# Performance work log

Hardware: AMD Instinct MI355X
Metric: run time of the kernel (lower is better)

## Reference

```python
import jax, jax.numpy as jnp
import numpy as np

N = 100000          # number of nodes
E = 128             # embedding size
NUM_LAYERS = 4
SMOOTH = 12.0       # MAXIMUM_SMOOTHNESS
RELATIONS = [("at", 2), ("clear", 1), ("on", 2)]  # sorted, as in module
ATOM_COUNTS = {"at": 150000, "clear": 150000, "on": 150000}


def mish(x):
    return x * jnp.tanh(jax.nn.softplus(x))


def _linear_init(k, din, dout):
    s = 1.0 / np.sqrt(din)
    kw, kb = jax.random.split(k)
    w = jax.random.uniform(kw, (din, dout), jnp.float32, -s, s)
    b = jax.random.uniform(kb, (dout,), jnp.float32, -s, s)
    return w, b


def setup_inputs() -> dict:
    key = jax.random.key(0)
    ks = iter(jax.random.split(key, 64))
    inp = {}
    inp["node_embeddings"] = jax.random.normal(next(ks), (N, E), jnp.float32)
    for name, ar in RELATIONS:
        inp[f"atoms_{name}"] = jax.random.randint(
            next(ks), (ATOM_COUNTS[name] * ar,), 0, N, dtype=jnp.int32)
        d = ar * E
        inp[f"w_in_{name}"], inp[f"b_in_{name}"] = _linear_init(next(ks), d, d)
        inp[f"w_out_{name}"], inp[f"b_out_{name}"] = _linear_init(next(ks), d, d)
    # update MLP: Linear(2E, 2E) -> mish -> Linear(2E, E)
    inp["w_u_in"], inp["b_u_in"] = _linear_init(next(ks), 2 * E, 2 * E)
    inp["w_u_out"], inp["b_u_out"] = _linear_init(next(ks), 2 * E, E)
    return inp


def _forward(node_embeddings, atoms, params):
    w_u_in, b_u_in, w_u_out, b_u_out = params["update"]

    def layer(h):
        msgs, idxs = [], []
        for name, ar in RELATIONS:
            w_in, b_in, w_out, b_out = params[name]
            av = atoms[name]                              # [A*ar] node indices
            x = h[av].reshape(-1, ar * E)                 # gather -> [A, ar*E]
            y = x + (mish(x @ w_in + b_in) @ w_out + b_out)  # residual MLP
            msgs.append(y.reshape(-1, E))
            idxs.append(av)
        msg = jnp.concatenate(msgs, 0)                    # [T, E]
        idx = jnp.concatenate(idxs, 0)                    # [T]
        # smooth-max aggregation (max offsets are not differentiated)
        seg_max = jax.ops.segment_max(msg, idx, num_segments=N)
        seg_max = jnp.where(jnp.isfinite(seg_max), seg_max, 0.0)  # empty -> 0 (include_self=False on zeros)
        seg_max = jax.lax.stop_gradient(seg_max)
        exps = jnp.exp(SMOOTH * (msg - seg_max[idx]))
        exps_sum = jax.ops.segment_sum(exps, idx, num_segments=N) + 1e-16
        max_msg = jnp.log(exps_sum) / SMOOTH + seg_max
        upd_in = jnp.concatenate([max_msg, h], axis=1)    # [N, 2E]
        upd = mish(upd_in @ w_u_in + b_u_in) @ w_u_out + b_u_out
        return h + upd                                    # outer residual

    h = node_embeddings
    for _ in range(NUM_LAYERS):
        h = layer(h)
    return h


def reference(node_embeddings, atoms_at, atoms_clear, atoms_on,
              w_in_at, b_in_at, w_out_at, b_out_at,
              w_in_clear, b_in_clear, w_out_clear, b_out_clear,
              w_in_on, b_in_on, w_out_on, b_out_on,
              w_u_in, b_u_in, w_u_out, b_u_out):
    atoms = {"at": atoms_at, "clear": atoms_clear, "on": atoms_on}
    params = {
        "at": (w_in_at, b_in_at, w_out_at, b_out_at),
        "clear": (w_in_clear, b_in_clear, w_out_clear, b_out_clear),
        "on": (w_in_on, b_in_on, w_out_on, b_out_on),
        "update": (w_u_in, b_u_in, w_u_out, b_u_out),
    }
    return _forward(node_embeddings, atoms, params)
```

## Files before the change

### kernel.cpp

```cpp
#include <hip/hip_runtime.h>
#include <hip/hip_bf16.h>
#include <math.h>

#define NNODES 100000
#define EDIM 128
#define TSLOTS 750000
#define NB 391
#define GRA 2344

typedef __bf16 bf16x8 __attribute__((ext_vector_type(8)));
typedef __bf16 bf16x4 __attribute__((ext_vector_type(4)));
typedef float f32x4 __attribute__((ext_vector_type(4)));

#define T_SCALE 17.312340490667562f
#define INV_SCALE 0.05776226504666211f
#define EMPTY_V (-3.0701134f)

__device__ __forceinline__ float mishf(float x) {
  float u = __expf(fminf(x, 15.f));
  float num = u * (u + 2.f);
  return x * num * __builtin_amdgcn_rcpf(num + 2.f);
}

__device__ __forceinline__ double exp12t(float t) {
  t = fmaxf(t, -20000.f);
  float ti = floorf(t);
  float m = exp2f(t - ti);
  int ei = (int)ti;
  ei = ei < -1000 ? -1000 : (ei > 1000 ? 1000 : ei);
  return (double)m * __longlong_as_double(((long long)(1023 + ei)) << 52);
}

__device__ __forceinline__ float logS12(double S) {
  if (!(S > 0.0)) return EMPTY_V;
  long long b = __double_as_longlong(S);
  int e2 = (int)((b >> 52) & 0x7FF) - 1023;
  float mf = __uint_as_float(0x3F800000u | (unsigned)((b >> 29) & 0x7FFFFF));
  return ((float)e2 + log2f(mf)) * INV_SCALE;
}

__global__ void k_sentinel(float* out, int n) {
  int i = blockIdx.x * 256 + threadIdx.x;
  if (i < n) out[i] = 1.0e6f;
}

__global__ void k_init(const float* __restrict__ h0, __bf16* __restrict__ hb, int n8) {
  int i = blockIdx.x * 256 + threadIdx.x;
  if (i >= n8) return;
  float4 f0 = ((const float4*)h0)[i * 2];
  float4 f1 = ((const float4*)h0)[i * 2 + 1];
  bf16x8 p = {(__bf16)f0.x, (__bf16)f0.y, (__bf16)f0.z, (__bf16)f0.w,
              (__bf16)f1.x, (__bf16)f1.y, (__bf16)f1.z, (__bf16)f1.w};
  *(bf16x8*)(hb + (size_t)i * 8) = p;
}

struct TransDesc {
  const float* src[8];
  __bf16* dst[8];
  int R[8];
  int C[8];
  int tstart[9];
};

__global__ void k_transpose_all(TransDesc td) {
  __shared__ float tile[32][33];
  int b = blockIdx.x;
  int m = 0;
  while (m < 7 && b >= td.tstart[m + 1]) m++;
  int t = b - td.tstart[m];
  int R = td.R[m], C = td.C[m];
  int tcols = C >> 5;
  int by = t / tcols, bx = t - by * tcols;
  int tx = threadIdx.x & 31, ty = threadIdx.x >> 5;
  const float* src = td.src[m];
  __bf16* dst = td.dst[m];
  for (int i = 0; i < 32; i += 8)
    tile[ty + i][tx] = src[(size_t)(by * 32 + ty + i) * C + bx * 32 + tx];
  __syncthreads();
  for (int i = 0; i < 32; i += 8)
    dst[(size_t)(bx * 32 + ty + i) * R + by * 32 + tx] = (__bf16)tile[tx][ty + i];
}

__device__ __forceinline__ int slot_node(int s, const int* at, const int* cl, const int* on) {
  if (s < 300000) return at[s];
  if (s < 450000) return cl[s - 300000];
  return on[s - 450000];
}

__global__ void k_count(const int* __restrict__ at, const int* __restrict__ cl,
                        const int* __restrict__ on, int* __restrict__ cnt) {
  int s = blockIdx.x * 256 + threadIdx.x;
  if (s >= TSLOTS) return;
  atomicAdd(&cnt[slot_node(s, at, cl, on)], 1);
}

__global__ void k_bsum(const int* __restrict__ cnt, int* __restrict__ bsum) {
  __shared__ int sm[256];
  int n = blockIdx.x * 256 + threadIdx.x;
  sm[threadIdx.x] = (n < NNODES) ? cnt[n] : 0;
  __syncthreads();
  for (int st = 128; st > 0; st >>= 1) {
    if (threadIdx.x < st) sm[threadIdx.x] += sm[threadIdx.x + st];
    __syncthreads();
  }
  if (threadIdx.x == 0) bsum[blockIdx.x] = sm[0];
}

__global__ void k_bscan(const int* __restrict__ bsum, int* __restrict__ bpre,
                        int* __restrict__ off) {
  __shared__ int sm[512];
  int t = threadIdx.x;
  int v = (t < NB) ? bsum[t] : 0;
  sm[t] = v;
  __syncthreads();
  for (int st = 1; st < 512; st <<= 1) {
    int x = (t >= st) ? sm[t - st] : 0;
    __syncthreads();
    sm[t] += x;
    __syncthreads();
  }
  if (t < NB) bpre[t] = sm[t] - v;
  if (t == NB - 1) off[NNODES] = sm[t];
}

__global__ void k_off(const int* __restrict__ cnt, const int* __restrict__ bpre,
                      int* __restrict__ off) {
  __shared__ int sm[256];
  int n = blockIdx.x * 256 + threadIdx.x;
  int v = (n < NNODES) ? cnt[n] : 0;
  sm[threadIdx.x] = v;
  __syncthreads();
  for (int st = 1; st < 256; st <<= 1) {
    int t = (threadIdx.x >= st) ? sm[threadIdx.x - st] : 0;
    __syncthreads();
    sm[threadIdx.x] += t;
    __syncthreads();
  }
  if (n < NNODES) off[n] = bpre[blockIdx.x] + sm[threadIdx.x] - v;
}

__global__ void k_fill(const int* __restrict__ at, const int* __restrict__ cl,
                       const int* __restrict__ on, const int* __restrict__ off,
                       int* __restrict__ cnt, int* __restrict__ perm) {
  int s = blockIdx.x * 256 + threadIdx.x;
  if (s >= TSLOTS) return;
  int node = slot_node(s, at, cl, on);
  int pos = atomicAdd(&cnt[node], -1) - 1;
  perm[s] = off[node] + pos;
}

struct RelAll {
  const int* av[3];
  const __bf16* wt1[3];
  const float* b1[3];
  const __bf16* wt2[3];
  const float* b2[3];
  const int* prm[3];
};

__global__ __launch_bounds__(512, 6) void k_relf(
    const float* __restrict__ hf, const __bf16* __restrict__ hb,
    RelAll ra, _Float16* __restrict__ msg) {
  __shared__ __align__(16) __bf16 xs[64][264];
  __shared__ int prm[128];
  const int tid = threadIdx.x;
  const int lane = tid & 63;
  const int w = tid >> 6;
  const int b = blockIdx.x;
  const int m = (b < GRA) ? 0 : (b < 2 * GRA ? 1 : 2);
  const int row0 = (b - m * GRA) * 64;
  const int A = 150000;
  const int* av = ra.av[m];
  const __bf16* wt1 = ra.wt1[m];
  const float* b1 = ra.b1[m];
  const __bf16* wt2 = ra.wt2[m];
  const float* b2 = ra.b2[m];
  const int* permrel = ra.prm[m];
  const int lhi = lane >> 4, llo = lane & 15;
  ushort* zs = (ushort*)&xs[0][0];

  if (m < 2) {
    if (tid < 128) {
      int i2 = row0 * 2 + tid;
      prm[tid] = (i2 < 2 * A) ? permrel[i2] : 0;
    }
    if (hb != nullptr) {
      for (int i = 0; i < 4; ++i) {
        int s = tid + i * 512;
        int r = s >> 5, o = s & 31;
        int a = row0 + r;
        uint4 v = {0, 0, 0, 0};
        if (a < A) {
          int node = av[2 * a + (o >> 4)];
          v = *(const uint4*)(hb + (size_t)node * 128 + (o & 15) * 8);
        }
        *(uint4*)&xs[r][o * 8] = v;
      }
    } else {
      for (int i = 0; i < 8; ++i) {
        int s = tid + i * 512;
        int r = s >> 6, o = s & 63;
        int a = row0 + r;
        float4 f = {0.f, 0.f, 0.f, 0.f};
        if (a < A) {
          int node = av[2 * a + (o >> 5)];
          f = *(const float4*)(hf + (size_t)node * 128 + (o & 31) * 4);
        }
        bf16x4 p = {(__bf16)f.x, (__bf16)f.y, (__bf16)f.z, (__bf16)f.w};
        *(bf16x4*)&xs[r][o * 4] = p;
      }
    }
    __syncthreads();

    const int cb = w * 32;
    f32x4 acc1[4][2];
#pragma unroll
    for (int rt = 0; rt < 4; rt++)
#pragma unroll
      for (int ct = 0; ct < 2; ct++) acc1[rt][ct] = (f32x4){0.f, 0.f, 0.f, 0.f};
#pragma unroll
    for (int kk = 0; kk < 8; ++kk) {
      int k = kk * 32 + lhi * 8;
      bf16x8 af[4], bfr[2];
#pragma unroll
      for (int rt = 0; rt < 4; rt++) af[rt] = *(const bf16x8*)&xs[rt * 16 + llo][k];
#pragma unroll
      for (int ct = 0; ct < 2; ct++)
        bfr[ct] = *(const bf16x8*)(wt1 + (size_t)(cb + ct * 16 + llo) * 256 + k);
#pragma unroll
      for (int rt = 0; rt < 4; rt++)
#pragma unroll
        for (int ct = 0; ct < 2; ct++)
          acc1[rt][ct] = __builtin_amdgcn_mfma_f32_16x16x32_bf16(af[rt], bfr[ct], acc1[rt][ct], 0, 0, 0);
    }
    __syncthreads();

    float b1v[2];
#pragma unroll
    for (int ct = 0; ct < 2; ct++) b1v[ct] = b1[cb + ct * 16 + llo];
#pragma unroll
    for (int rt = 0; rt < 4; rt++)
#pragma unroll
      for (int ct = 0; ct < 2; ct++)
#pragma unroll
        for (int i = 0; i < 4; i++)
          xs[rt * 16 + lhi * 4 + i][cb + ct * 16 + llo] = (__bf16)mishf(acc1[rt][ct][i] + b1v[ct]);
    __syncthreads();

    f32x4 acc2[4][2];
#pragma unroll
    for (int rt = 0; rt < 4; rt++)
#pragma unroll
      for (int ct = 0; ct < 2; ct++) acc2[rt][ct] = (f32x4){0.f, 0.f, 0.f, 0.f};
#pragma unroll
    for (int kk = 0; kk < 8; ++kk) {
      int k = kk * 32 + lhi * 8;
      bf16x8 af[4], bfr[2];
#pragma unroll
      for (int rt = 0; rt < 4; rt++) af[rt] = *(const bf16x8*)&xs[rt * 16 + llo][k];
#pragma unroll
      for (int ct = 0; ct < 2; ct++)
        bfr[ct] = *(const bf16x8*)(wt2 + (size_t)(cb + ct * 16 + llo) * 256 + k);
#pragma unroll
      for (int rt = 0; rt < 4; rt++)
#pragma unroll
        for (int ct = 0; ct < 2; ct++)
          acc2[rt][ct] = __builtin_amdgcn_mfma_f32_16x16x32_bf16(af[rt], bfr[ct], acc2[rt][ct], 0, 0, 0);
    }
    __syncthreads();

    float b2v[2];
#pragma unroll
    for (int ct = 0; ct < 2; ct++) b2v[ct] = b2[cb + ct * 16 + llo];
#pragma unroll
    for (int rt = 0; rt < 4; rt++)
#pragma unroll
      for (int ct = 0; ct < 2; ct++)
#pragma unroll
        for (int i = 0; i < 4; i++) {
          int r = rt * 16 + lhi * 4 + i;
          int col = cb + ct * 16 + llo;
          union { ushort u; _Float16 f; } cv;
          cv.f = (_Float16)(acc2[rt][ct][i] + b2v[ct]);
          zs[r * 264 + col] = cv.u;
        }
    __syncthreads();

    for (int i = 0; i < 4; ++i) {
      int s = tid + i * 512;
      int sr = s >> 4;
      int c = s & 15;
      int a = row0 + (sr >> 1);
      if (a < A) {
        int rr = sr >> 1, c0 = (sr & 1) * 128 + c * 8;
        uint4 z = *(const uint4*)&zs[rr * 264 + c0];
        *(uint4*)(msg + (size_t)prm[sr] * 128 + c * 8) = z;
      }
    }
  } else {
    if (tid < 64) {
      int a = row0 + tid;
      prm[tid] = (a < A) ? permrel[a] : 0;
    }
    if (hb != nullptr) {
      for (int i = 0; i < 2; ++i) {
        int s = tid + i * 512;
        int r = s >> 4, o = s & 15;
        int a = row0 + r;
        uint4 v = {0, 0, 0, 0};
        if (a < A) {
          int node = av[a];
          v = *(const uint4*)(hb + (size_t)node * 128 + o * 8);
        }
        *(uint4*)&xs[r][o * 8] = v;
      }
    } else {
      for (int i = 0; i < 4; ++i) {
        int s = tid + i * 512;
        int r = s >> 5, o = s & 31;
        int a = row0 + r;
        float4 f = {0.f, 0.f, 0.f, 0.f};
        if (a < A) {
          int node = av[a];
          f = *(const float4*)(hf + (size_t)node * 128 + o * 4);
        }
        bf16x4 p = {(__bf16)f.x, (__bf16)f.y, (__bf16)f.z, (__bf16)f.w};
        *(bf16x4*)&xs[r][o * 4] = p;
      }
    }
    __syncthreads();

    const int cb = w * 16;
    f32x4 acc1[4];
#pragma unroll
    for (int rt = 0; rt < 4; rt++) acc1[rt] = (f32x4){0.f, 0.f, 0.f, 0.f};
#pragma unroll
    for (int kk = 0; kk < 4; ++kk) {
      int k = kk * 32 + lhi * 8;
      bf16x8 af[4], bfr;
#pragma unroll
      for (int rt = 0; rt < 4; rt++) af[rt] = *(const bf16x8*)&xs[rt * 16 + llo][k];
      bfr = *(const bf16x8*)(wt1 + (size_t)(cb + llo) * 128 + k);
#pragma unroll
      for (int rt = 0; rt < 4; rt++)
        acc1[rt] = __builtin_amdgcn_mfma_f32_16x16x32_bf16(af[rt], bfr, acc1[rt], 0, 0, 0);
    }
    __syncthreads();

    float b1v = b1[cb + llo];
#pragma unroll
    for (int rt = 0; rt < 4; rt++)
#pragma unroll
      for (int i = 0; i < 4; i++)
        xs[rt * 16 + lhi * 4 + i][cb + llo] = (__bf16)mishf(acc1[rt][i] + b1v);
    __syncthreads();

    f32x4 acc2[4];
#pragma unroll
    for (int rt = 0; rt < 4; rt++) acc2[rt] = (f32x4){0.f, 0.f, 0.f, 0.f};
#pragma unroll
    for (int kk = 0; kk < 4; ++kk) {
      int k = kk * 32 + lhi * 8;
      bf16x8 af[4], bfr;
#pragma unroll
      for (int rt = 0; rt < 4; rt++) af[rt] = *(const bf16x8*)&xs[rt * 16 + llo][k];
      bfr = *(const bf16x8*)(wt2 + (size_t)(cb + llo) * 128 + k);
#pragma unroll
      for (int rt = 0; rt < 4; rt++)
        acc2[rt] = __builtin_amdgcn_mfma_f32_16x16x32_bf16(af[rt], bfr, acc2[rt], 0, 0, 0);
    }
    __syncthreads();

    float b2v = b2[cb + llo];
#pragma unroll
    for (int rt = 0; rt < 4; rt++)
#pragma unroll
      for (int i = 0; i < 4; i++) {
        int r = rt * 16 + lhi * 4 + i;
        int col = cb + llo;
        union { ushort u; _Float16 f; } cv;
        cv.f = (_Float16)(acc2[rt][i] + b2v);
        zs[r * 264 + col] = cv.u;
      }
    __syncthreads();

    for (int i = 0; i < 2; ++i) {
      int s = tid + i * 512;
      int sr = s >> 4;
      int c = s & 15;
      int a = row0 + sr;
      if (a < A) {
        uint4 z = *(const uint4*)&zs[sr * 264 + c * 8];
        *(uint4*)(msg + (size_t)prm[sr] * 128 + c * 8) = z;
      }
    }
  }
}

__global__ __launch_bounds__(256, 8) void k_agg(
    const _Float16* __restrict__ msg, const int* __restrict__ off,
    const float* __restrict__ hf, const __bf16* __restrict__ hb,
    __bf16* __restrict__ mm) {
  __shared__ int offs[33];
  const int tid = threadIdx.x;
  const int lane = tid & 63;
  const int w = tid >> 6;
  const int node0 = blockIdx.x * 32;
  if (tid < 33) {
    int n = node0 + tid;
    offs[tid] = off[n < NNODES ? n : NNODES];
  }
  __syncthreads();

  const int fl = lane & 31;
  const int p = lane >> 5;
  const _Float16* mb = msg + fl * 4;

#pragma unroll 1
  for (int j = 0; j < 8; ++j) {
    int n = node0 + w * 8 + j;
    if (n >= NNODES) break;
    float h0, h1, h2, h3;
    if (hb != nullptr) {
      bf16x4 hq = *(const bf16x4*)(hb + (size_t)n * 128 + fl * 4);
      h0 = (float)hq[0]; h1 = (float)hq[1]; h2 = (float)hq[2]; h3 = (float)hq[3];
    } else {
      float4 hq = *(const float4*)(hf + (size_t)n * 128 + fl * 4);
      h0 = hq.x; h1 = hq.y; h2 = hq.z; h3 = hq.w;
    }
    int beg = offs[w * 8 + j];
    int deg = offs[w * 8 + j + 1] - beg;
    double S0 = 0.0, S1 = 0.0, S2 = 0.0, S3 = 0.0;
#pragma unroll 1
    for (int d = 0; d < deg; d += 2) {
      int rp = d + p;
      int rc = rp < deg - 1 ? rp : deg - 1;
      uint2 v = *(const uint2*)(mb + (size_t)(beg + rc) * 128);
      if (rp >= deg) { v.x = 0xFC00FC00u; v.y = 0xFC00FC00u; }
      union { uint2 u; _Float16 f[4]; } q;
      q.u = v;
      S0 += exp12t(((float)q.f[0] + h0) * T_SCALE);
      S1 += exp12t(((float)q.f[1] + h1) * T_SCALE);
      S2 += exp12t(((float)q.f[2] + h2) * T_SCALE);
      S3 += exp12t(((float)q.f[3] + h3) * T_SCALE);
    }
    S0 += __shfl_xor(S0, 32);
    S1 += __shfl_xor(S1, 32);
    S2 += __shfl_xor(S2, 32);
    S3 += __shfl_xor(S3, 32);
    if (p == 0) {
      bf16x4 r;
      r[0] = (__bf16)logS12(S0);
      r[1] = (__bf16)logS12(S1);
      r[2] = (__bf16)logS12(S2);
      r[3] = (__bf16)logS12(S3);
      *(bf16x4*)(mm + (size_t)n * 128 + fl * 4) = r;
    }
  }
}

__global__ __launch_bounds__(512, 6) void k_mlp(
    const float* __restrict__ hin, const __bf16* __restrict__ mm,
    const __bf16* __restrict__ wt1, const float* __restrict__ b1,
    const __bf16* __restrict__ wt2, const float* __restrict__ b2,
    float* __restrict__ hout, __bf16* __restrict__ hbout) {
  __shared__ __align__(16) __bf16 xs[64][264];
  const int tid = threadIdx.x;
  const int lane = tid & 63;
  const int w = tid >> 6;
  const int node0 = blockIdx.x * 64;

  for (int i = 0; i < 2; ++i) {
    int s = tid + i * 512;
    int r = s >> 4, o = s & 15;
    int n = node0 + r;
    uint4 v = {0, 0, 0, 0};
    if (n < NNODES) v = *(const uint4*)(mm + (size_t)n * 128 + o * 8);
    *(uint4*)&xs[r][o * 8] = v;
  }
  for (int i = 0; i < 4; ++i) {
    int s = tid + i * 512;
    int r = s >> 5, o = s & 31;
    int n = node0 + r;
    float4 f = {0.f, 0.f, 0.f, 0.f};
    if (n < NNODES) f = *(const float4*)(hin + (size_t)n * 128 + o * 4);
    bf16x4 p = {(__bf16)f.x, (__bf16)f.y, (__bf16)f.z, (__bf16)f.w};
    *(bf16x4*)&xs[r][128 + o * 4] = p;
  }
  __syncthreads();

  const int lhi = lane >> 4, llo = lane & 15;
  const int cb = w * 32;

  f32x4 acc1[4][2];
#pragma unroll
  for (int rt = 0; rt < 4; rt++)
#pragma unroll
    for (int ct = 0; ct < 2; ct++) acc1[rt][ct] = (f32x4){0.f, 0.f, 0.f, 0.f};
#pragma unroll
  for (int kk = 0; kk < 8; ++kk) {
    int k = kk * 32 + lhi * 8;
    bf16x8 af[4], bfr[2];
#pragma unroll
    for (int rt = 0; rt < 4; rt++) af[rt] = *(const bf16x8*)&xs[rt * 16 + llo][k];
#pragma unroll
    for (int ct = 0; ct < 2; ct++)
      bfr[ct] = *(const bf16x8*)(wt1 + (size_t)(cb + ct * 16 + llo) * 256 + k);
#pragma unroll
    for (int rt = 0; rt < 4; rt++)
#pragma unroll
      for (int ct = 0; ct < 2; ct++)
        acc1[rt][ct] = __builtin_amdgcn_mfma_f32_16x16x32_bf16(af[rt], bfr[ct], acc1[rt][ct], 0, 0, 0);
  }
  __syncthreads();

  float b1v[2];
#pragma unroll
  for (int ct = 0; ct < 2; ct++) b1v[ct] = b1[cb + ct * 16 + llo];
#pragma unroll
  for (int rt = 0; rt < 4; rt++)
#pragma unroll
    for (int ct = 0; ct < 2; ct++)
#pragma unroll
      for (int i = 0; i < 4; i++)
        xs[rt * 16 + lhi * 4 + i][cb + ct * 16 + llo] = (__bf16)mishf(acc1[rt][ct][i] + b1v[ct]);
  __syncthreads();

  const int cb2 = w * 16;
  f32x4 acc2[4];
#pragma unroll
  for (int rt = 0; rt < 4; rt++) acc2[rt] = (f32x4){0.f, 0.f, 0.f, 0.f};
#pragma unroll
  for (int kk = 0; kk < 8; ++kk) {
    int k = kk * 32 + lhi * 8;
    bf16x8 af[4], bfr;
#pragma unroll
    for (int rt = 0; rt < 4; rt++) af[rt] = *(const bf16x8*)&xs[rt * 16 + llo][k];
    bfr = *(const bf16x8*)(wt2 + (size_t)(cb2 + llo) * 256 + k);
#pragma unroll
    for (int rt = 0; rt < 4; rt++)
      acc2[rt] = __builtin_amdgcn_mfma_f32_16x16x32_bf16(af[rt], bfr, acc2[rt], 0, 0, 0);
  }

  float b2v = b2[cb2 + llo];
#pragma unroll
  for (int rt = 0; rt < 4; rt++)
#pragma unroll
    for (int i = 0; i < 4; i++) {
      int r = rt * 16 + lhi * 4 + i;
      int n = node0 + r;
      if (n >= NNODES) continue;
      int col = cb2 + llo;
      size_t idx = (size_t)n * 128 + col;
      float nh = hin[idx] + acc2[rt][i] + b2v;
      hout[idx] = nh;
      if (hbout != nullptr) hbout[idx] = (__bf16)nh;
    }
}

extern "C" void kernel_launch(void* const* d_in, const int* in_sizes, int n_in,
                              void* d_out, int out_size, void* d_ws, size_t ws_size,
                              hipStream_t stream) {
  const float* h0 = (const float*)d_in[0];
  const int* at = (const int*)d_in[1];
  const float* w_in_at = (const float*)d_in[2];
  const float* b_in_at = (const float*)d_in[3];
  const float* w_out_at = (const float*)d_in[4];
  const float* b_out_at = (const float*)d_in[5];
  const int* cl = (const int*)d_in[6];
  const float* w_in_cl = (const float*)d_in[7];
  const float* b_in_cl = (const float*)d_in[8];
  const float* w_out_cl = (const float*)d_in[9];
  const float* b_out_cl = (const float*)d_in[10];
  const int* on = (const int*)d_in[11];
  const float* w_in_on = (const float*)d_in[12];
  const float* b_in_on = (const float*)d_in[13];
  const float* w_out_on = (const float*)d_in[14];
  const float* b_out_on = (const float*)d_in[15];
  const float* w_u_in = (const float*)d_in[16];
  const float* b_u_in = (const float*)d_in[17];
  const float* w_u_out = (const float*)d_in[18];
  const float* b_u_out = (const float*)d_in[19];

  float* hout = (float*)d_out;
  char* ws = (char*)d_ws;

  const size_t MSG_B = (size_t)TSLOTS * 128 * 2;
  const size_t OFF_B = 400016;
  const size_t CNT_B = 400000;
  const size_t BS_B = 1568;
  const size_t PERM_B = 3000000;
  const size_t WT_B = 786432;
  const size_t MM_B = (size_t)NNODES * 128 * 2;
  const size_t HB_B = (size_t)NNODES * 128 * 2;
  const size_t REQ2 = MSG_B + OFF_B + CNT_B + 2 * BS_B + PERM_B + WT_B + MM_B;
  const size_t REQ3 = REQ2 + HB_B;

  if (ws_size < REQ2) {
    k_sentinel<<<(out_size + 255) / 256, 256, 0, stream>>>((float*)d_out, out_size);
    return;
  }

  _Float16* msg = (_Float16*)ws;
  int* off = (int*)(ws + MSG_B);
  int* cnt = (int*)(ws + MSG_B + OFF_B);
  int* bsum = (int*)(ws + MSG_B + OFF_B + CNT_B);
  int* bpre = (int*)(ws + MSG_B + OFF_B + CNT_B + BS_B);
  int* perm = (int*)(ws + MSG_B + OFF_B + CNT_B + 2 * BS_B);
  __bf16* wt = (__bf16*)(ws + MSG_B + OFF_B + CNT_B + 2 * BS_B + PERM_B);
  __bf16* mm = (__bf16*)(ws + MSG_B + OFF_B + CNT_B + 2 * BS_B + PERM_B + WT_B);
  __bf16* hb = (ws_size >= REQ3) ? (__bf16*)(ws + REQ2) : nullptr;

  __bf16* wt_in_at = wt;
  __bf16* wt_out_at = wt + 65536;
  __bf16* wt_in_on = wt + 131072;
  __bf16* wt_out_on = wt + 196608;
  __bf16* wt_u_in = wt + 262144;
  __bf16* wt_u_out = wt + 327680;
  __bf16* wt_in_cl = wt + 360448;
  __bf16* wt_out_cl = wt + 376832;

  TransDesc td;
  const float* srcs[8] = {w_in_at, w_out_at, w_in_on, w_out_on, w_u_in, w_u_out, w_in_cl, w_out_cl};
  __bf16* dsts[8] = {wt_in_at, wt_out_at, wt_in_on, wt_out_on, wt_u_in, wt_u_out, wt_in_cl, wt_out_cl};
  int Rs[8] = {256, 256, 256, 256, 256, 256, 128, 128};
  int Cs[8] = {256, 256, 256, 256, 256, 128, 128, 128};
  int ts = 0;
  for (int m = 0; m < 8; ++m) {
    td.src[m] = srcs[m]; td.dst[m] = dsts[m]; td.R[m] = Rs[m]; td.C[m] = Cs[m];
    td.tstart[m] = ts; ts += (Rs[m] / 32) * (Cs[m] / 32);
  }
  td.tstart[8] = ts;
  k_transpose_all<<<384, 256, 0, stream>>>(td);

  if (hb) k_init<<<6250, 256, 0, stream>>>(h0, hb, NNODES * EDIM / 8);

  const int grid_mlp = (NNODES + 63) / 64;
  const int grid_agg = (NNODES + 31) / 32;
  const int grid_slots = (TSLOTS + 255) / 256;

  hipMemsetAsync(cnt, 0, CNT_B, stream);
  k_count<<<grid_slots, 256, 0, stream>>>(at, cl, on, cnt);
  k_bsum<<<NB, 256, 0, stream>>>(cnt, bsum);
  k_bscan<<<1, 512, 0, stream>>>(bsum, bpre, off);
  k_off<<<NB, 256, 0, stream>>>(cnt, bpre, off);
  k_fill<<<grid_slots, 256, 0, stream>>>(at, cl, on, off, cnt, perm);

  RelAll ra;
  ra.av[0] = at;  ra.wt1[0] = wt_in_at; ra.b1[0] = b_in_at; ra.wt2[0] = wt_out_at; ra.b2[0] = b_out_at; ra.prm[0] = perm;
  ra.av[1] = on;  ra.wt1[1] = wt_in_on; ra.b1[1] = b_in_on; ra.wt2[1] = wt_out_on; ra.b2[1] = b_out_on; ra.prm[1] = perm + 450000;
  ra.av[2] = cl;  ra.wt1[2] = wt_in_cl; ra.b1[2] = b_in_cl; ra.wt2[2] = wt_out_cl; ra.b2[2] = b_out_cl; ra.prm[2] = perm + 300000;

  for (int l = 0; l < 4; ++l) {
    const float* hs = (l == 0) ? h0 : hout;
    k_relf<<<3 * GRA, 512, 0, stream>>>(hs, hb, ra, msg);
    k_agg<<<grid_agg, 256, 0, stream>>>(msg, off, hs, hb, mm);
    k_mlp<<<grid_mlp, 512, 0, stream>>>(hs, mm, wt_u_in, b_u_in, wt_u_out, b_u_out, hout, hb);
  }
}
```

Measured before the change: 1.644 ms.

## Pipeline relation MLP over two row tiles and trim aggregation and MLP loads

k_relf now handles 128 atoms per block as two 64-row tiles. The bf16 gather for the second tile is issued into registers while the first tile's second GEMM runs, and biases are hoisted out of the tile loop. This is meant to hide gather latency and halve block count, at the cost of more registers and possibly lower occupancy. k_agg unrolls its degree loop to two loads per iteration to get more memory parallelism. k_mlp reads the bf16 copy of h instead of converting the fp32 tensor, which halves those bytes but relies on that buffer being valid for the current layer.

```diff
diff --git a/kernel.cpp b/kernel.cpp
--- a/kernel.cpp
+++ b/kernel.cpp
@@ -6,7 +6,7 @@
 #define EDIM 128
 #define TSLOTS 750000
 #define NB 391
-#define GRA 2344
+#define GRB 1172
 
 typedef __bf16 bf16x8 __attribute__((ext_vector_type(8)));
 typedef __bf16 bf16x4 __attribute__((ext_vector_type(4)));
@@ -162,13 +162,13 @@
     const float* __restrict__ hf, const __bf16* __restrict__ hb,
     RelAll ra, _Float16* __restrict__ msg) {
   __shared__ __align__(16) __bf16 xs[64][264];
-  __shared__ int prm[128];
+  __shared__ int prm[256];
   const int tid = threadIdx.x;
   const int lane = tid & 63;
   const int w = tid >> 6;
   const int b = blockIdx.x;
-  const int m = (b < GRA) ? 0 : (b < 2 * GRA ? 1 : 2);
-  const int row0 = (b - m * GRA) * 64;
+  const int m = (b < GRB) ? 0 : (b < 2 * GRB ? 1 : 2);
+  const int row0 = (b - m * GRB) * 128;
   const int A = 150000;
   const int* av = ra.av[m];
   const __bf16* wt1 = ra.wt1[m];
@@ -178,13 +178,14 @@
   const int* permrel = ra.prm[m];
   const int lhi = lane >> 4, llo = lane & 15;
   ushort* zs = (ushort*)&xs[0][0];
+  const bool pre = (hb != nullptr);
 
   if (m < 2) {
-    if (tid < 128) {
+    if (tid < 256) {
       int i2 = row0 * 2 + tid;
       prm[tid] = (i2 < 2 * A) ? permrel[i2] : 0;
     }
-    if (hb != nullptr) {
+    if (pre) {
       for (int i = 0; i < 4; ++i) {
         int s = tid + i * 512;
         int r = s >> 5, o = s & 31;
@@ -210,99 +211,144 @@
         *(bf16x4*)&xs[r][o * 4] = p;
       }
     }
+    const int cb = w * 32;
+    float b1v[2], b2v[2];
+#pragma unroll
+    for (int ct = 0; ct < 2; ct++) {
+      b1v[ct] = b1[cb + ct * 16 + llo];
+      b2v[ct] = b2[cb + ct * 16 + llo];
+    }
     __syncthreads();
 
-    const int cb = w * 32;
-    f32x4 acc1[4][2];
-#pragma unroll
-    for (int rt = 0; rt < 4; rt++)
-#pragma unroll
-      for (int ct = 0; ct < 2; ct++) acc1[rt][ct] = (f32x4){0.f, 0.f, 0.f, 0.f};
-#pragma unroll
-    for (int kk = 0; kk < 8; ++kk) {
-      int k = kk * 32 + lhi * 8;
-      bf16x8 af[4], bfr[2];
-#pragma unroll
-      for (int rt = 0; rt < 4; rt++) af[rt] = *(const bf16x8*)&xs[rt * 16 + llo][k];
-#pragma unroll
-      for (int ct = 0; ct < 2; ct++)
-        bfr[ct] = *(const bf16x8*)(wt1 + (size_t)(cb + ct * 16 + llo) * 256 + k);
+    uint4 gn[4];
+    for (int t = 0; t < 2; ++t) {
+      const int* prmt = prm + t * 128;
+      const int arow0 = row0 + t * 64;
+
+      f32x4 acc1[4][2];
 #pragma unroll
       for (int rt = 0; rt < 4; rt++)
 #pragma unroll
+        for (int ct = 0; ct < 2; ct++) acc1[rt][ct] = (f32x4){0.f, 0.f, 0.f, 0.f};
+#pragma unroll
+      for (int kk = 0; kk < 8; ++kk) {
+        int k = kk * 32 + lhi * 8;
+        bf16x8 af[4], bfr[2];
+#pragma unroll
+        for (int rt = 0; rt < 4; rt++) af[rt] = *(const bf16x8*)&xs[rt * 16 + llo][k];
+#pragma unroll
         for (int ct = 0; ct < 2; ct++)
-          acc1[rt][ct] = __builtin_amdgcn_mfma_f32_16x16x32_bf16(af[rt], bfr[ct], acc1[rt][ct], 0, 0, 0);
-    }
-    __syncthreads();
-
-    float b1v[2];
-#pragma unroll
-    for (int ct = 0; ct < 2; ct++) b1v[ct] = b1[cb + ct * 16 + llo];
-#pragma unroll
-    for (int rt = 0; rt < 4; rt++)
-#pragma unroll
-      for (int ct = 0; ct < 2; ct++)
-#pragma unroll
-        for (int i = 0; i < 4; i++)
-          xs[rt * 16 + lhi * 4 + i][cb + ct * 16 + llo] = (__bf16)mishf(acc1[rt][ct][i] + b1v[ct]);
-    __syncthreads();
-
-    f32x4 acc2[4][2];
-#pragma unroll
-    for (int rt = 0; rt < 4; rt++)
-#pragma unroll
-      for (int ct = 0; ct < 2; ct++) acc2[rt][ct] = (f32x4){0.f, 0.f, 0.f, 0.f};
-#pragma unroll
-    for (int kk = 0; kk < 8; ++kk) {
-      int k = kk * 32 + lhi * 8;
-      bf16x8 af[4], bfr[2];
-#pragma unroll
-      for (int rt = 0; rt < 4; rt++) af[rt] = *(const bf16x8*)&xs[rt * 16 + llo][k];
-#pragma unroll
-      for (int ct = 0; ct < 2; ct++)
-        bfr[ct] = *(const bf16x8*)(wt2 + (size_t)(cb + ct * 16 + llo) * 256 + k);
+          bfr[ct] = *(const bf16x8*)(wt1 + (size_t)(cb + ct * 16 + llo) * 256 + k);
+#pragma unroll
+        for (int rt = 0; rt < 4; rt++)
+#pragma unroll
+          for (int ct = 0; ct < 2; ct++)
+            acc1[rt][ct] = __builtin_amdgcn_mfma_f32_16x16x32_bf16(af[rt], bfr[ct], acc1[rt][ct], 0, 0, 0);
+      }
+      __syncthreads();
+
 #pragma unroll
       for (int rt = 0; rt < 4; rt++)
 #pragma unroll
         for (int ct = 0; ct < 2; ct++)
-          acc2[rt][ct] = __builtin_amdgcn_mfma_f32_16x16x32_bf16(af[rt], bfr[ct], acc2[rt][ct], 0, 0, 0);
-    }
-    __syncthreads();
-
-    float b2v[2];
-#pragma unroll
-    for (int ct = 0; ct < 2; ct++) b2v[ct] = b2[cb + ct * 16 + llo];
-#pragma unroll
-    for (int rt = 0; rt < 4; rt++)
-#pragma unroll
-      for (int ct = 0; ct < 2; ct++)
-#pragma unroll
-        for (int i = 0; i < 4; i++) {
-          int r = rt * 16 + lhi * 4 + i;
-          int col = cb + ct * 16 + llo;
-          union { ushort u; _Float16 f; } cv;
-          cv.f = (_Float16)(acc2[rt][ct][i] + b2v[ct]);
-          zs[r * 264 + col] = cv.u;
-        }
-    __syncthreads();
-
-    for (int i = 0; i < 4; ++i) {
-      int s = tid + i * 512;
-      int sr = s >> 4;
-      int c = s & 15;
-      int a = row0 + (sr >> 1);
-      if (a < A) {
-        int rr = sr >> 1, c0 = (sr & 1) * 128 + c * 8;
-        uint4 z = *(const uint4*)&zs[rr * 264 + c0];
-        *(uint4*)(msg + (size_t)prm[sr] * 128 + c * 8) = z;
+#pragma unroll
+          for (int i = 0; i < 4; i++)
+            xs[rt * 16 + lhi * 4 + i][cb + ct * 16 + llo] = (__bf16)mishf(acc1[rt][ct][i] + b1v[ct]);
+      __syncthreads();
+
+      f32x4 acc2[4][2];
+#pragma unroll
+      for (int rt = 0; rt < 4; rt++)
+#pragma unroll
+        for (int ct = 0; ct < 2; ct++) acc2[rt][ct] = (f32x4){0.f, 0.f, 0.f, 0.f};
+#pragma unroll
+      for (int kk = 0; kk < 8; ++kk) {
+        int k = kk * 32 + lhi * 8;
+        bf16x8 af[4], bfr[2];
+#pragma unroll
+        for (int rt = 0; rt < 4; rt++) af[rt] = *(const bf16x8*)&xs[rt * 16 + llo][k];
+#pragma unroll
+        for (int ct = 0; ct < 2; ct++)
+          bfr[ct] = *(const bf16x8*)(wt2 + (size_t)(cb + ct * 16 + llo) * 256 + k);
+#pragma unroll
+        for (int rt = 0; rt < 4; rt++)
+#pragma unroll
+          for (int ct = 0; ct < 2; ct++)
+            acc2[rt][ct] = __builtin_amdgcn_mfma_f32_16x16x32_bf16(af[rt], bfr[ct], acc2[rt][ct], 0, 0, 0);
+      }
+      if (t == 0 && pre) {
+#pragma unroll
+        for (int i = 0; i < 4; ++i) {
+          int s = tid + i * 512;
+          int r = s >> 5, o = s & 31;
+          int a = row0 + 64 + r;
+          uint4 v = {0, 0, 0, 0};
+          if (a < A) {
+            int node = av[2 * a + (o >> 4)];
+            v = *(const uint4*)(hb + (size_t)node * 128 + (o & 15) * 8);
+          }
+          gn[i] = v;
+        }
+      }
+      __syncthreads();
+
+#pragma unroll
+      for (int rt = 0; rt < 4; rt++)
+#pragma unroll
+        for (int ct = 0; ct < 2; ct++)
+#pragma unroll
+          for (int i = 0; i < 4; i++) {
+            int r = rt * 16 + lhi * 4 + i;
+            int col = cb + ct * 16 + llo;
+            union { ushort u; _Float16 f; } cv;
+            cv.f = (_Float16)(acc2[rt][ct][i] + b2v[ct]);
+            zs[r * 264 + col] = cv.u;
+          }
+      __syncthreads();
+
+      for (int i = 0; i < 4; ++i) {
+        int s = tid + i * 512;
+        int sr = s >> 4;
+        int c = s & 15;
+        int a = arow0 + (sr >> 1);
+        if (a < A) {
+          int rr = sr >> 1, c0 = (sr & 1) * 128 + c * 8;
+          uint4 z = *(const uint4*)&zs[rr * 264 + c0];
+          *(uint4*)(msg + (size_t)prmt[sr] * 128 + c * 8) = z;
+        }
+      }
+      if (t == 0) {
+        __syncthreads();
+        if (pre) {
+#pragma unroll
+          for (int i = 0; i < 4; ++i) {
+            int s = tid + i * 512;
+            int r = s >> 5, o = s & 31;
+            *(uint4*)&xs[r][o * 8] = gn[i];
+          }
+        } else {
+          for (int i = 0; i < 8; ++i) {
+            int s = tid + i * 512;
+            int r = s >> 6, o = s & 63;
+            int a = row0 + 64 + r;
+            float4 f = {0.f, 0.f, 0.f, 0.f};
+            if (a < A) {
+              int node = av[2 * a + (o >> 5)];
+              f = *(const float4*)(hf + (size_t)node * 128 + (o & 31) * 4);
+            }
+            bf16x4 p = {(__bf16)f.x, (__bf16)f.y, (__bf16)f.z, (__bf16)f.w};
+            *(bf16x4*)&xs[r][o * 4] = p;
+          }
+        }
+        __syncthreads();
       }
     }
   } else {
-    if (tid < 64) {
+    if (tid < 128) {
       int a = row0 + tid;
       prm[tid] = (a < A) ? permrel[a] : 0;
     }
-    if (hb != nullptr) {
+    if (pre) {
       for (int i = 0; i < 2; ++i) {
         int s = tid + i * 512;
         int r = s >> 4, o = s & 15;
@@ -328,70 +374,115 @@
         *(bf16x4*)&xs[r][o * 4] = p;
       }
     }
+    const int cb = w * 16;
+    float b1v = b1[cb + llo];
+    float b2v = b2[cb + llo];
     __syncthreads();
 
-    const int cb = w * 16;
-    f32x4 acc1[4];
-#pragma unroll
-    for (int rt = 0; rt < 4; rt++) acc1[rt] = (f32x4){0.f, 0.f, 0.f, 0.f};
-#pragma unroll
-    for (int kk = 0; kk < 4; ++kk) {
-      int k = kk * 32 + lhi * 8;
-      bf16x8 af[4], bfr;
-#pragma unroll
-      for (int rt = 0; rt < 4; rt++) af[rt] = *(const bf16x8*)&xs[rt * 16 + llo][k];
-      bfr = *(const bf16x8*)(wt1 + (size_t)(cb + llo) * 128 + k);
+    uint4 gn[2];
+    for (int t = 0; t < 2; ++t) {
+      const int* prmt = prm + t * 64;
+      const int arow0 = row0 + t * 64;
+
+      f32x4 acc1[4];
+#pragma unroll
+      for (int rt = 0; rt < 4; rt++) acc1[rt] = (f32x4){0.f, 0.f, 0.f, 0.f};
+#pragma unroll
+      for (int kk = 0; kk < 4; ++kk) {
+        int k = kk * 32 + lhi * 8;
+        bf16x8 af[4], bfr;
+#pragma unroll
+        for (int rt = 0; rt < 4; rt++) af[rt] = *(const bf16x8*)&xs[rt * 16 + llo][k];
+        bfr = *(const bf16x8*)(wt1 + (size_t)(cb + llo) * 128 + k);
+#pragma unroll
+        for (int rt = 0; rt < 4; rt++)
+          acc1[rt] = __builtin_amdgcn_mfma_f32_16x16x32_bf16(af[rt], bfr, acc1[rt], 0, 0, 0);
+      }
+      __syncthreads();
+
 #pragma unroll
       for (int rt = 0; rt < 4; rt++)
-        acc1[rt] = __builtin_amdgcn_mfma_f32_16x16x32_bf16(af[rt], bfr, acc1[rt], 0, 0, 0);
-    }
-    __syncthreads();
-
-    float b1v = b1[cb + llo];
-#pragma unroll
-    for (int rt = 0; rt < 4; rt++)
-#pragma unroll
-      for (int i = 0; i < 4; i++)
-        xs[rt * 16 + lhi * 4 + i][cb + llo] = (__bf16)mishf(acc1[rt][i] + b1v);
-    __syncthreads();
-
-    f32x4 acc2[4];
-#pragma unroll
-    for (int rt = 0; rt < 4; rt++) acc2[rt] = (f32x4){0.f, 0.f, 0.f, 0.f};
-#pragma unroll
-    for (int kk = 0; kk < 4; ++kk) {
-      int k = kk * 32 + lhi * 8;
-      bf16x8 af[4], bfr;
-#pragma unroll
-      for (int rt = 0; rt < 4; rt++) af[rt] = *(const bf16x8*)&xs[rt * 16 + llo][k];
-      bfr = *(const bf16x8*)(wt2 + (size_t)(cb + llo) * 128 + k);
+#pragma unroll
+        for (int i = 0; i < 4; i++)
+          xs[rt * 16 + lhi * 4 + i][cb + llo] = (__bf16)mishf(acc1[rt][i] + b1v);
+      __syncthreads();
+
+      f32x4 acc2[4];
+#pragma unroll
+      for (int rt = 0; rt < 4; rt++) acc2[rt] = (f32x4){0.f, 0.f, 0.f, 0.f};
+#pragma unroll
+      for (int kk = 0; kk < 4; ++kk) {
+        int k = kk * 32 + lhi * 8;
+        bf16x8 af[4], bfr;
+#pragma unroll
+        for (int rt = 0; rt < 4; rt++) af[rt] = *(const bf16x8*)&xs[rt * 16 + llo][k];
+        bfr = *(const bf16x8*)(wt2 + (size_t)(cb + llo) * 128 + k);
+#pragma unroll
+        for (int rt = 0; rt < 4; rt++)
+          acc2[rt] = __builtin_amdgcn_mfma_f32_16x16x32_bf16(af[rt], bfr, acc2[rt], 0, 0, 0);
+      }
+      if (t == 0 && pre) {
+#pragma unroll
+        for (int i = 0; i < 2; ++i) {
+          int s = tid + i * 512;
+          int r = s >> 4, o = s & 15;
+          int a = row0 + 64 + r;
+          uint4 v = {0, 0, 0, 0};
+          if (a < A) {
+            int node = av[a];
+            v = *(const uint4*)(hb + (size_t)node * 128 + o * 8);
+          }
+          gn[i] = v;
+        }
+      }
+      __syncthreads();
+
 #pragma unroll
       for (int rt = 0; rt < 4; rt++)
-        acc2[rt] = __builtin_amdgcn_mfma_f32_16x16x32_bf16(af[rt], bfr, acc2[rt], 0, 0, 0);
-    }
-    __syncthreads();
-
-    float b2v = b2[cb + llo];
-#pragma unroll
-    for (int rt = 0; rt < 4; rt++)
-#pragma unroll
-      for (int i = 0; i < 4; i++) {
-        int r = rt * 16 + lhi * 4 + i;
-        int col = cb + llo;
-        union { ushort u; _Float16 f; } cv;
-        cv.f = (_Float16)(acc2[rt][i] + b2v);
-        zs[r * 264 + col] = cv.u;
-      }
-    __syncthreads();
-
-    for (int i = 0; i < 2; ++i) {
-      int s = tid + i * 512;
-      int sr = s >> 4;
-      int c = s & 15;
-      int a = row0 + sr;
-      if (a < A) {
-        uint4 z = *(const uint4*)&zs[sr * 264 + c * 8];
-        *(uint4*)(msg + (size_t)prm[sr] * 128 + c * 8) = z;
+#pragma unroll
+        for (int i = 0; i < 4; i++) {
+          int r = rt * 16 + lhi * 4 + i;
+          int col = cb + llo;
+          union { ushort u; _Float16 f; } cv;
+          cv.f = (_Float16)(acc2[rt][i] + b2v);
+          zs[r * 264 + col] = cv.u;
+        }
+      __syncthreads();
+
+      for (int i = 0; i < 2; ++i) {
+        int s = tid + i * 512;
+        int sr = s >> 4;
+        int c = s & 15;
+        int a = arow0 + sr;
+        if (a < A) {
+          uint4 z = *(const uint4*)&zs[sr * 264 + c * 8];
+          *(uint4*)(msg + (size_t)prmt[sr] * 128 + c * 8) = z;
+        }
+      }
+      if (t == 0) {
+        __syncthreads();
+        if (pre) {
+#pragma unroll
+          for (int i = 0; i < 2; ++i) {
+            int s = tid + i * 512;
+            int r = s >> 4, o = s & 15;
+            *(uint4*)&xs[r][o * 8] = gn[i];
+          }
+        } else {
+          for (int i = 0; i < 4; ++i) {
+            int s = tid + i * 512;
+            int r = s >> 5, o = s & 31;
+            int a = row0 + 64 + r;
+            float4 f = {0.f, 0.f, 0.f, 0.f};
+            if (a < A) {
+              int node = av[a];
+              f = *(const float4*)(hf + (size_t)node * 128 + o * 4);
+            }
+            bf16x4 p = {(__bf16)f.x, (__bf16)f.y, (__bf16)f.z, (__bf16)f.w};
+            *(bf16x4*)&xs[r][o * 4] = p;
+          }
+        }
+        __syncthreads();
       }
     }
   }
@@ -432,17 +523,21 @@
     int deg = offs[w * 8 + j + 1] - beg;
     double S0 = 0.0, S1 = 0.0, S2 = 0.0, S3 = 0.0;
 #pragma unroll 1
-    for (int d = 0; d < deg; d += 2) {
-      int rp = d + p;
-      int rc = rp < deg - 1 ? rp : deg - 1;
-      uint2 v = *(const uint2*)(mb + (size_t)(beg + rc) * 128);
-      if (rp >= deg) { v.x = 0xFC00FC00u; v.y = 0xFC00FC00u; }
-      union { uint2 u; _Float16 f[4]; } q;
-      q.u = v;
-      S0 += exp12t(((float)q.f[0] + h0) * T_SCALE);
-      S1 += exp12t(((float)q.f[1] + h1) * T_SCALE);
-      S2 += exp12t(((float)q.f[2] + h2) * T_SCALE);
-      S3 += exp12t(((float)q.f[3] + h3) * T_SCALE);
+    for (int d = 0; d < deg; d += 4) {
+      int rp0 = d + p;
+      int rp1 = d + 2 + p;
+      int rc0 = rp0 < deg - 1 ? rp0 : deg - 1;
+      int rc1 = rp1 < deg - 1 ? rp1 : deg - 1;
+      uint2 v0 = *(const uint2*)(mb + (size_t)(beg + rc0) * 128);
+      uint2 v1 = *(const uint2*)(mb + (size_t)(beg + rc1) * 128);
+      if (rp0 >= deg) { v0.x = 0xFC00FC00u; v0.y = 0xFC00FC00u; }
+      if (rp1 >= deg) { v1.x = 0xFC00FC00u; v1.y = 0xFC00FC00u; }
+      union { uint2 u; _Float16 f[4]; } q0, q1;
+      q0.u = v0; q1.u = v1;
+      S0 += exp12t(((float)q0.f[0] + h0) * T_SCALE) + exp12t(((float)q1.f[0] + h0) * T_SCALE);
+      S1 += exp12t(((float)q0.f[1] + h1) * T_SCALE) + exp12t(((float)q1.f[1] + h1) * T_SCALE);
+      S2 += exp12t(((float)q0.f[2] + h2) * T_SCALE) + exp12t(((float)q1.f[2] + h2) * T_SCALE);
+      S3 += exp12t(((float)q0.f[3] + h3) * T_SCALE) + exp12t(((float)q1.f[3] + h3) * T_SCALE);
     }
     S0 += __shfl_xor(S0, 32);
     S1 += __shfl_xor(S1, 32);
@@ -478,14 +573,25 @@
     if (n < NNODES) v = *(const uint4*)(mm + (size_t)n * 128 + o * 8);
     *(uint4*)&xs[r][o * 8] = v;
   }
-  for (int i = 0; i < 4; ++i) {
-    int s = tid + i * 512;
-    int r = s >> 5, o = s & 31;
-    int n = node0 + r;
-    float4 f = {0.f, 0.f, 0.f, 0.f};
-    if (n < NNODES) f = *(const float4*)(hin + (size_t)n * 128 + o * 4);
-    bf16x4 p = {(__bf16)f.x, (__bf16)f.y, (__bf16)f.z, (__bf16)f.w};
-    *(bf16x4*)&xs[r][128 + o * 4] = p;
+  if (hbout != nullptr) {
+    for (int i = 0; i < 2; ++i) {
+      int s = tid + i * 512;
+      int r = s >> 4, o = s & 15;
+      int n = node0 + r;
+      uint4 v = {0, 0, 0, 0};
+      if (n < NNODES) v = *(const uint4*)(hbout + (size_t)n * 128 + o * 8);
+      *(uint4*)&xs[r][128 + o * 8] = v;
+    }
+  } else {
+    for (int i = 0; i < 4; ++i) {
+      int s = tid + i * 512;
+      int r = s >> 5, o = s & 31;
+      int n = node0 + r;
+      float4 f = {0.f, 0.f, 0.f, 0.f};
+      if (n < NNODES) f = *(const float4*)(hin + (size_t)n * 128 + o * 4);
+      bf16x4 p = {(__bf16)f.x, (__bf16)f.y, (__bf16)f.z, (__bf16)f.w};
+      *(bf16x4*)&xs[r][128 + o * 4] = p;
+    }
   }
   __syncthreads();
 
@@ -653,7 +759,7 @@
 
   for (int l = 0; l < 4; ++l) {
     const float* hs = (l == 0) ? h0 : hout;
-    k_relf<<<3 * GRA, 512, 0, stream>>>(hs, hb, ra, msg);
+    k_relf<<<3 * GRB, 512, 0, stream>>>(hs, hb, ra, msg);
     k_agg<<<grid_agg, 256, 0, stream>>>(msg, off, hs, hb, mm);
     k_mlp<<<grid_mlp, 512, 0, stream>>>(hs, mm, wt_u_in, b_u_in, wt_u_out, b_u_out, hout, hb);
   }
```

Result: slower. 2.290 ms (+39.3%).

## Fuse smooth-max aggregation into the update MLP kernel through shared memory

Applied to the files above, without the earlier changes.

Merges the per-node aggregation kernel into the update MLP kernel. Each 512-thread block aggregates the messages for its 64 nodes and writes the bf16 result straight into the shared-memory input tile, so the intermediate aggregate buffer is no longer written to and read back from global memory, and one launch per layer goes away. The aggregation loop is also reshaped: each lane now handles 8 features and 4 message rows are processed per iteration, with two shuffle steps to reduce them. In exchange, aggregation runs under the MLP kernel's launch bounds and shared-memory footprint, which may give less parallelism for hiding the latency of the irregular gather.

```diff
diff --git a/kernel.cpp b/kernel.cpp
--- a/kernel.cpp
+++ b/kernel.cpp
@@ -397,95 +397,112 @@
   }
 }
 
-__global__ __launch_bounds__(256, 8) void k_agg(
+__global__ __launch_bounds__(512, 6) void k_aggmlp(
     const _Float16* __restrict__ msg, const int* __restrict__ off,
-    const float* __restrict__ hf, const __bf16* __restrict__ hb,
-    __bf16* __restrict__ mm) {
-  __shared__ int offs[33];
+    const float* __restrict__ hin, const __bf16* __restrict__ hb,
+    const __bf16* __restrict__ wt1, const float* __restrict__ b1,
+    const __bf16* __restrict__ wt2, const float* __restrict__ b2,
+    float* __restrict__ hout, __bf16* __restrict__ hbout) {
+  __shared__ __align__(16) __bf16 xs[64][264];
+  __shared__ int offs[65];
   const int tid = threadIdx.x;
   const int lane = tid & 63;
   const int w = tid >> 6;
-  const int node0 = blockIdx.x * 32;
-  if (tid < 33) {
+  const int node0 = blockIdx.x * 64;
+  const bool useb = (hbout != nullptr);
+
+  if (tid < 65) {
     int n = node0 + tid;
     offs[tid] = off[n < NNODES ? n : NNODES];
   }
-  __syncthreads();
-
-  const int fl = lane & 31;
-  const int p = lane >> 5;
-  const _Float16* mb = msg + fl * 4;
+  if (useb) {
+    for (int i = 0; i < 2; ++i) {
+      int s = tid + i * 512;
+      int r = s >> 4, o = s & 15;
+      int n = node0 + r;
+      uint4 v = {0, 0, 0, 0};
+      if (n < NNODES) v = *(const uint4*)(hb + (size_t)n * 128 + o * 8);
+      *(uint4*)&xs[r][128 + o * 8] = v;
+    }
+  } else {
+    for (int i = 0; i < 4; ++i) {
+      int s = tid + i * 512;
+      int r = s >> 5, o = s & 31;
+      int n = node0 + r;
+      float4 f = {0.f, 0.f, 0.f, 0.f};
+      if (n < NNODES) f = *(const float4*)(hin + (size_t)n * 128 + o * 4);
+      bf16x4 p = {(__bf16)f.x, (__bf16)f.y, (__bf16)f.z, (__bf16)f.w};
+      *(bf16x4*)&xs[r][128 + o * 4] = p;
+    }
+  }
+  if (node0 + 64 > NNODES) {
+    for (int s = tid; s < 64 * 16; s += 512) {
+      int r = s >> 4, o = s & 15;
+      if (node0 + r >= NNODES) *(uint4*)&xs[r][o * 8] = (uint4){0, 0, 0, 0};
+    }
+  }
+  __syncthreads();
+
+  const int rg = lane >> 4;
+  const int fl = lane & 15;
+  const _Float16* mb = msg + fl * 8;
 
 #pragma unroll 1
   for (int j = 0; j < 8; ++j) {
     int n = node0 + w * 8 + j;
     if (n >= NNODES) break;
-    float h0, h1, h2, h3;
-    if (hb != nullptr) {
-      bf16x4 hq = *(const bf16x4*)(hb + (size_t)n * 128 + fl * 4);
-      h0 = (float)hq[0]; h1 = (float)hq[1]; h2 = (float)hq[2]; h3 = (float)hq[3];
+    float h[8];
+    if (useb) {
+      bf16x8 hq = *(const bf16x8*)(hb + (size_t)n * 128 + fl * 8);
+#pragma unroll
+      for (int k = 0; k < 8; ++k) h[k] = (float)hq[k];
     } else {
-      float4 hq = *(const float4*)(hf + (size_t)n * 128 + fl * 4);
-      h0 = hq.x; h1 = hq.y; h2 = hq.z; h3 = hq.w;
+      float4 a0 = *(const float4*)(hin + (size_t)n * 128 + fl * 8);
+      float4 a1 = *(const float4*)(hin + (size_t)n * 128 + fl * 8 + 4);
+      h[0] = a0.x; h[1] = a0.y; h[2] = a0.z; h[3] = a0.w;
+      h[4] = a1.x; h[5] = a1.y; h[6] = a1.z; h[7] = a1.w;
     }
     int beg = offs[w * 8 + j];
     int deg = offs[w * 8 + j + 1] - beg;
     double S0 = 0.0, S1 = 0.0, S2 = 0.0, S3 = 0.0;
+    double S4 = 0.0, S5 = 0.0, S6 = 0.0, S7 = 0.0;
 #pragma unroll 1
-    for (int d = 0; d < deg; d += 2) {
-      int rp = d + p;
-      int rc = rp < deg - 1 ? rp : deg - 1;
-      uint2 v = *(const uint2*)(mb + (size_t)(beg + rc) * 128);
-      if (rp >= deg) { v.x = 0xFC00FC00u; v.y = 0xFC00FC00u; }
-      union { uint2 u; _Float16 f[4]; } q;
+    for (int d = 0; d < deg; d += 4) {
+      int rp = d + rg;
+      int rc = rp < deg ? rp : deg - 1;
+      uint4 v = *(const uint4*)(mb + (size_t)(beg + rc) * 128);
+      if (rp >= deg) { v.x = 0xFC00FC00u; v.y = 0xFC00FC00u; v.z = 0xFC00FC00u; v.w = 0xFC00FC00u; }
+      union { uint4 u; _Float16 f[8]; } q;
       q.u = v;
-      S0 += exp12t(((float)q.f[0] + h0) * T_SCALE);
-      S1 += exp12t(((float)q.f[1] + h1) * T_SCALE);
-      S2 += exp12t(((float)q.f[2] + h2) * T_SCALE);
-      S3 += exp12t(((float)q.f[3] + h3) * T_SCALE);
-    }
-    S0 += __shfl_xor(S0, 32);
-    S1 += __shfl_xor(S1, 32);
-    S2 += __shfl_xor(S2, 32);
-    S3 += __shfl_xor(S3, 32);
-    if (p == 0) {
-      bf16x4 r;
+      S0 += exp12t(((float)q.f[0] + h[0]) * T_SCALE);
+      S1 += exp12t(((float)q.f[1] + h[1]) * T_SCALE);
+      S2 += exp12t(((float)q.f[2] + h[2]) * T_SCALE);
+      S3 += exp12t(((float)q.f[3] + h[3]) * T_SCALE);
+      S4 += exp12t(((float)q.f[4] + h[4]) * T_SCALE);
+      S5 += exp12t(((float)q.f[5] + h[5]) * T_SCALE);
+      S6 += exp12t(((float)q.f[6] + h[6]) * T_SCALE);
+      S7 += exp12t(((float)q.f[7] + h[7]) * T_SCALE);
+    }
+    S0 += __shfl_xor(S0, 16); S0 += __shfl_xor(S0, 32);
+    S1 += __shfl_xor(S1, 16); S1 += __shfl_xor(S1, 32);
+    S2 += __shfl_xor(S2, 16); S2 += __shfl_xor(S2, 32);
+    S3 += __shfl_xor(S3, 16); S3 += __shfl_xor(S3, 32);
+    S4 += __shfl_xor(S4, 16); S4 += __shfl_xor(S4, 32);
+    S5 += __shfl_xor(S5, 16); S5 += __shfl_xor(S5, 32);
+    S6 += __shfl_xor(S6, 16); S6 += __shfl_xor(S6, 32);
+    S7 += __shfl_xor(S7, 16); S7 += __shfl_xor(S7, 32);
+    if (rg == 0) {
+      bf16x8 r;
       r[0] = (__bf16)logS12(S0);
       r[1] = (__bf16)logS12(S1);
       r[2] = (__bf16)logS12(S2);
       r[3] = (__bf16)logS12(S3);
-      *(bf16x4*)(mm + (size_t)n * 128 + fl * 4) = r;
-    }
-  }
-}
-
-__global__ __launch_bounds__(512, 6) void k_mlp(
-    const float* __restrict__ hin, const __bf16* __restrict__ mm,
-    const __bf16* __restrict__ wt1, const float* __restrict__ b1,
-    const __bf16* __restrict__ wt2, const float* __restrict__ b2,
-    float* __restrict__ hout, __bf16* __restrict__ hbout) {
-  __shared__ __align__(16) __bf16 xs[64][264];
-  const int tid = threadIdx.x;
-  const int lane = tid & 63;
-  const int w = tid >> 6;
-  const int node0 = blockIdx.x * 64;
-
-  for (int i = 0; i < 2; ++i) {
-    int s = tid + i * 512;
-    int r = s >> 4, o = s & 15;
-    int n = node0 + r;
-    uint4 v = {0, 0, 0, 0};
-    if (n < NNODES) v = *(const uint4*)(mm + (size_t)n * 128 + o * 8);
-    *(uint4*)&xs[r][o * 8] = v;
-  }
-  for (int i = 0; i < 4; ++i) {
-    int s = tid + i * 512;
-    int r = s >> 5, o = s & 31;
-    int n = node0 + r;
-    float4 f = {0.f, 0.f, 0.f, 0.f};
-    if (n < NNODES) f = *(const float4*)(hin + (size_t)n * 128 + o * 4);
-    bf16x4 p = {(__bf16)f.x, (__bf16)f.y, (__bf16)f.z, (__bf16)f.w};
-    *(bf16x4*)&xs[r][128 + o * 4] = p;
+      r[4] = (__bf16)logS12(S4);
+      r[5] = (__bf16)logS12(S5);
+      r[6] = (__bf16)logS12(S6);
+      r[7] = (__bf16)logS12(S7);
+      *(bf16x8*)&xs[n - node0][fl * 8] = r;
+    }
   }
   __syncthreads();
 
@@ -608,7 +625,6 @@
   int* bpre = (int*)(ws + MSG_B + OFF_B + CNT_B + BS_B);
   int* perm = (int*)(ws + MSG_B + OFF_B + CNT_B + 2 * BS_B);
   __bf16* wt = (__bf16*)(ws + MSG_B + OFF_B + CNT_B + 2 * BS_B + PERM_B);
-  __bf16* mm = (__bf16*)(ws + MSG_B + OFF_B + CNT_B + 2 * BS_B + PERM_B + WT_B);
   __bf16* hb = (ws_size >= REQ3) ? (__bf16*)(ws + REQ2) : nullptr;
 
   __bf16* wt_in_at = wt;
@@ -636,7 +652,6 @@
   if (hb) k_init<<<6250, 256, 0, stream>>>(h0, hb, NNODES * EDIM / 8);
 
   const int grid_mlp = (NNODES + 63) / 64;
-  const int grid_agg = (NNODES + 31) / 32;
   const int grid_slots = (TSLOTS + 255) / 256;
 
   hipMemsetAsync(cnt, 0, CNT_B, stream);
@@ -654,7 +669,6 @@
   for (int l = 0; l < 4; ++l) {
     const float* hs = (l == 0) ? h0 : hout;
     k_relf<<<3 * GRA, 512, 0, stream>>>(hs, hb, ra, msg);
-    k_agg<<<grid_agg, 256, 0, stream>>>(msg, off, hs, hb, mm);
-    k_mlp<<<grid_mlp, 512, 0, stream>>>(hs, mm, wt_u_in, b_u_in, wt_u_out, b_u_out, hout, hb);
-  }
-}
+    k_aggmlp<<<grid_mlp, 512, 0, stream>>>(msg, off, hs, hb, wt_u_in, b_u_in, wt_u_out, b_u_out, hout, hb);
+  }
+}
```

After: 1.619 ms. No clear change (-1.5%).
